# Performance work log

Measured on AMD Instinct MI355X. Metric: run time of the kernel, lower is better.

## Reference

```python
import jax, jax.numpy as jnp
import numpy as np

EMB_DIM = 256
Q_DIM = 512
V_DIM = 512

def setup_inputs() -> dict:
    key = jax.random.key(0)
    ks = jax.random.split(key, 7)
    B, S = 8, 2048
    x = jax.random.normal(ks[0], (B, S, EMB_DIM), dtype=jnp.float32)
    s = 1.0 / np.sqrt(EMB_DIM)
    Wq = jax.random.normal(ks[1], (EMB_DIM, Q_DIM), dtype=jnp.float32) * s
    bq = jax.random.normal(ks[2], (Q_DIM,), dtype=jnp.float32) * 0.01
    Wk = jax.random.normal(ks[3], (EMB_DIM, Q_DIM), dtype=jnp.float32) * s
    bk = jax.random.normal(ks[4], (Q_DIM,), dtype=jnp.float32) * 0.01
    Wv = jax.random.normal(ks[5], (EMB_DIM, V_DIM), dtype=jnp.float32) * s
    bv = jax.random.normal(ks[6], (V_DIM,), dtype=jnp.float32) * 0.01
    return {"x": x, "Wq": Wq, "bq": bq, "Wk": Wk, "bk": bk, "Wv": Wv, "bv": bv}

def reference(x, Wq, bq, Wk, bk, Wv, bv):
    # q/k/v projections (torch Linear == x @ W + b with W stored [in, out] here)
    q = jax.nn.sigmoid(jnp.einsum('bse,eq->bsq', x, Wq) + bq)   # [B,S,Q]
    k = jnp.einsum('bse,eq->bsq', x, Wk) + bk                   # [B,S,Q]
    v = jnp.einsum('bse,ev->bsv', x, Wv) + bv                   # [B,S,V]
    scale = 1.0 / jnp.sqrt(jnp.float32(EMB_DIM))
    qk = jnp.einsum('bsq,btq->bst', q, k) * scale               # [B,S,S]
    qk = jax.nn.elu(qk)
    attn = jax.nn.softmax(qk, axis=-1)
    return jnp.einsum('bst,btv->bsv', attn, v)                  # [B,S,V]
```

## Files before the change

kernel.cpp:

```cpp
#include <hip/hip_runtime.h>
#include <hip/hip_bf16.h>
#include <math.h>

typedef unsigned short u16;
using short8 = __attribute__((ext_vector_type(8))) short;
using f32x4  = __attribute__((ext_vector_type(4))) float;

#define BK 32


__device__ __forceinline__ u16 f2bf(float f) {
  union { float f; unsigned u; } v; v.f = f;
  unsigned r = v.u + 0x7FFFu + ((v.u >> 16) & 1u);
  return (u16)(r >> 16);
}

__device__ __forceinline__ float fexp(float x) { return __expf(x); }

__device__ __forceinline__ void gld16(const void* g, void* l) {
  __builtin_amdgcn_global_load_lds(
      (const __attribute__((address_space(1))) void*)g,
      (__attribute__((address_space(3))) void*)l,
      16, 0, 0);
}


__device__ __forceinline__ void gemm_core64(const u16* __restrict__ Ag,
                                            const u16* __restrict__ Bg,
                                            int K, int lda, int ldb,
                                            u16* As, u16* Bs,
                                            f32x4 acc[4][4], int w, int l) {
  const int wm = (w & 1) << 6, wn = (w >> 1) << 6;
  const int ln = l & 15, lq = l >> 4;
  const int sr0 = w * 16 + (l >> 2);
  const int sr1 = 64 + sr0;
  const int skp = (l & 3) * 8;
  const int skg = ((l & 3) ^ ((l >> 3) & 3)) * 8;
  const int kro = (lq ^ ((ln >> 1) & 3)) * 8;

#pragma unroll
  for (int mt = 0; mt < 4; mt++)
#pragma unroll
    for (int nt = 0; nt < 4; nt++) acc[mt][nt] = (f32x4)0.0f;

  for (int k0 = 0; k0 < K; k0 += 64) {
    __syncthreads();
    gld16(Ag + (size_t)sr0 * lda + k0 + skg, As + sr0 * BK + skp);
    gld16(Ag + (size_t)sr1 * lda + k0 + skg, As + sr1 * BK + skp);
    gld16(Ag + (size_t)sr0 * lda + k0 + 32 + skg, As + 4096 + sr0 * BK + skp);
    gld16(Ag + (size_t)sr1 * lda + k0 + 32 + skg, As + 4096 + sr1 * BK + skp);
    gld16(Bg + (size_t)sr0 * ldb + k0 + skg, Bs + sr0 * BK + skp);
    gld16(Bg + (size_t)sr1 * ldb + k0 + skg, Bs + sr1 * BK + skp);
    gld16(Bg + (size_t)sr0 * ldb + k0 + 32 + skg, Bs + 4096 + sr0 * BK + skp);
    gld16(Bg + (size_t)sr1 * ldb + k0 + 32 + skg, Bs + 4096 + sr1 * BK + skp);
    __syncthreads();
#pragma unroll
    for (int h = 0; h < 2; h++) {
      const u16* Ah = As + h * 4096;
      const u16* Bh = Bs + h * 4096;
      short8 af[4], bf[4];
#pragma unroll
      for (int mt = 0; mt < 4; mt++)
        af[mt] = *(const short8*)(Ah + (wm + mt * 16 + ln) * BK + kro);
#pragma unroll
      for (int nt = 0; nt < 4; nt++)
        bf[nt] = *(const short8*)(Bh + (wn + nt * 16 + ln) * BK + kro);
#pragma unroll
      for (int mt = 0; mt < 4; mt++)
#pragma unroll
        for (int nt = 0; nt < 4; nt++)
          acc[mt][nt] = __builtin_amdgcn_mfma_f32_16x16x32_bf16(
              af[mt], bf[nt], acc[mt][nt], 0, 0, 0);
    }
  }
}


__global__ __launch_bounds__(256) void k_conv(
    const float* __restrict__ Wq, const float* __restrict__ Wk,
    const float* __restrict__ Wv, const float* __restrict__ bq,
    const float* __restrict__ bk, const float* __restrict__ bv,
    u16* __restrict__ Wt, float* __restrict__ bcat,
    float* __restrict__ lsum) {
  const int bid = blockIdx.x;
  if (bid < 1536) {
    int i = bid * 256 + threadIdx.x;
    int nn = i >> 8, e = i & 255;
    int sel = nn >> 9, c = nn & 511;
    const float* W = (sel == 0) ? Wq : (sel == 1) ? Wk : Wv;
    Wt[i] = f2bf(W[e * 512 + c]);
    if (e == 0) {
      const float* bb = (sel == 0) ? bq : (sel == 1) ? bk : bv;
      bcat[nn] = bb[c];
    }
  } else {
    int i = (bid - 1536) * 256 + threadIdx.x;
    lsum[i] = 0.0f;
  }
}


__global__ __launch_bounds__(256) void k_proj(
    const float* __restrict__ x, const u16* __restrict__ Wt,
    const float* __restrict__ bcat, u16* __restrict__ qb,
    u16* __restrict__ kb, u16* __restrict__ vtb) {
  __shared__ __align__(16) u16 As8[8 * 4096];
  __shared__ __align__(16) u16 Bs[2 * 4096];
  const int bm = blockIdx.y * 128;
  const int bnq = blockIdx.x;
  const int tid = threadIdx.x, w = tid >> 6, l = tid & 63;
  const int wm = (w & 1) << 6, wn = (w >> 1) << 6;
  const int ln = l & 15, lq = l >> 4;
  const int sr0 = w * 16 + (l >> 2);
  const int sr1 = 64 + sr0;
  const int skp = (l & 3) * 8;
  const int skg = ((l & 3) ^ ((l >> 3) & 3)) * 8;
  const int kro = (lq ^ ((ln >> 1) & 3)) * 8;

#pragma unroll
  for (int kw = 0; kw < 8; kw++) {
    const f32x4* s0 = (const f32x4*)(x + (size_t)(bm + sr0) * 256 + kw * 32 + skg);
    const f32x4* s1 = (const f32x4*)(x + (size_t)(bm + sr1) * 256 + kw * 32 + skg);
    f32x4 a0 = __builtin_nontemporal_load(s0);
    f32x4 a1 = __builtin_nontemporal_load(s0 + 1);
    f32x4 b0 = __builtin_nontemporal_load(s1);
    f32x4 b1 = __builtin_nontemporal_load(s1 + 1);
    short8 v0, v1;
#pragma unroll
    for (int j = 0; j < 4; j++) {
      ((u16*)&v0)[j]     = f2bf(a0[j]);
      ((u16*)&v0)[4 + j] = f2bf(a1[j]);
      ((u16*)&v1)[j]     = f2bf(b0[j]);
      ((u16*)&v1)[4 + j] = f2bf(b1[j]);
    }
    *(short8*)(As8 + kw * 4096 + sr0 * BK + skp) = v0;
    *(short8*)(As8 + kw * 4096 + sr1 * BK + skp) = v1;
  }

  const int b = bm >> 11, t0 = bm & 2047;
  const int cb = bnq * 128;

  for (int p = 0; p < 3; p++) {
    const u16* Bg = Wt + (size_t)(p * 512 + cb) * 256;
    f32x4 acc[4][4];
#pragma unroll
    for (int mt = 0; mt < 4; mt++)
#pragma unroll
      for (int nt = 0; nt < 4; nt++) acc[mt][nt] = (f32x4)0.0f;

#pragma unroll
    for (int it2 = 0; it2 < 4; it2++) {
      __syncthreads();
      gld16(Bg + (size_t)sr0 * 256 + it2 * 64 + skg, Bs + sr0 * BK + skp);
      gld16(Bg + (size_t)sr1 * 256 + it2 * 64 + skg, Bs + sr1 * BK + skp);
      gld16(Bg + (size_t)sr0 * 256 + it2 * 64 + 32 + skg,
            Bs + 4096 + sr0 * BK + skp);
      gld16(Bg + (size_t)sr1 * 256 + it2 * 64 + 32 + skg,
            Bs + 4096 + sr1 * BK + skp);
      __syncthreads();
#pragma unroll
      for (int h = 0; h < 2; h++) {
        const u16* Aw = As8 + (it2 * 2 + h) * 4096;
        const u16* Bh = Bs + h * 4096;
        short8 af[4], bf[4];
#pragma unroll
        for (int mt = 0; mt < 4; mt++)
          af[mt] = *(const short8*)(Aw + (wm + mt * 16 + ln) * BK + kro);
#pragma unroll
        for (int nt = 0; nt < 4; nt++)
          bf[nt] = *(const short8*)(Bh + (wn + nt * 16 + ln) * BK + kro);
#pragma unroll
        for (int mt = 0; mt < 4; mt++)
#pragma unroll
          for (int nt = 0; nt < 4; nt++)
            acc[mt][nt] = __builtin_amdgcn_mfma_f32_16x16x32_bf16(
                af[mt], bf[nt], acc[mt][nt], 0, 0, 0);
      }
    }

    if (p < 2) {
      u16* dst = p ? kb : qb;
#pragma unroll
      for (int mt = 0; mt < 4; mt++)
#pragma unroll
        for (int r = 0; r < 4; r++) {
          int row = bm + wm + mt * 16 + lq * 4 + r;
          ushort4 o;
#pragma unroll
          for (int nt = 0; nt < 4; nt++) {
            int col = wn + nt * 16 + ln;
            float v = acc[mt][nt][r] + bcat[p * 512 + cb + col];
            float ov = (p == 0) ? __builtin_amdgcn_rcpf(1.0f + fexp(-v)) : v;
            ((u16*)&o)[nt] = f2bf(ov);
          }
          *(ushort4*)&dst[(size_t)row * 512 + cb + wn + ln * 4] = o;
        }
    } else {
      u16* tr = As8;
#pragma unroll
      for (int h = 0; h < 2; h++) {
        __syncthreads();
        if ((w & 1) == h) {
#pragma unroll
          for (int nt = 0; nt < 4; nt++) {
            int c = wn + nt * 16 + ln;
            float bias = bcat[1024 + cb + c];
#pragma unroll
            for (int r = 0; r < 4; r++) {
              ushort4 o;
#pragma unroll
              for (int mm = 0; mm < 4; mm++)
                ((u16*)&o)[mm] = f2bf(acc[mm][nt][r] + bias);
              *(ushort4*)&tr[c * 68 + lq * 16 + r * 4] = o;
            }
          }
        }
        __syncthreads();
        int c2 = tid >> 1, half = tid & 1;
        size_t dbase = ((size_t)b * 512 + cb + c2) * 2048 + t0 + h * 64 + half * 32;
#pragma unroll
        for (int j = 0; j < 4; j++) {
          ushort4 a0 = *(const ushort4*)&tr[c2 * 68 + half * 32 + j * 8];
          ushort4 a1 = *(const ushort4*)&tr[c2 * 68 + half * 32 + j * 8 + 4];
          *(ushort4*)&vtb[dbase + j * 8] = a0;
          *(ushort4*)&vtb[dbase + j * 8 + 4] = a1;
        }
      }
    }
  }
}


__global__ __launch_bounds__(256, 4) void k_qk(const u16* __restrict__ qb,
                                               const u16* __restrict__ kb,
                                               u16* __restrict__ P,
                                               float* __restrict__ lsum) {
  __shared__ __align__(16) u16 As[2 * 4096];
  __shared__ __align__(16) u16 Bs[2 * 4096];
  const int bid = blockIdx.x;
  const int b = bid & 7, t = bid >> 3;
  const int bm = (t >> 4) * 128, bn = (t & 15) * 128;
  const size_t ob = (size_t)b * 2048 * 512;
  const int tid = threadIdx.x, w = tid >> 6, l = tid & 63;
  f32x4 acc[4][4];
  gemm_core64(qb + ob + (size_t)bm * 512, kb + ob + (size_t)bn * 512,
              512, 512, 512, As, Bs, acc, w, l);

  const int wm = (w & 1) << 6, wn = (w >> 1) << 6;
  const int ln = l & 15, lq = l >> 4;
  const float scale = 0.0625f;
#pragma unroll
  for (int mt = 0; mt < 4; mt++)
#pragma unroll
    for (int r = 0; r < 4; r++) {
      int row = bm + wm + mt * 16 + lq * 4 + r;
      float s = 0.0f;
      ushort4 o;
#pragma unroll
      for (int nt = 0; nt < 4; nt++) {
        float v = acc[mt][nt][r] * scale;
        float e = (v > 0.0f) ? v : (fexp(v) - 1.0f);
        float p = fexp(e);
        ((u16*)&o)[nt] = f2bf(p);
        s += p;
      }
      *(ushort4*)&P[((size_t)b * 2048 + row) * 2048 + bn + wn + ln * 4] = o;
#pragma unroll
      for (int o2 = 1; o2 < 16; o2 <<= 1) s += __shfl_xor(s, o2);
      if (ln == 0) atomicAdd(&lsum[b * 2048 + row], s);
    }
}


__global__ __launch_bounds__(256, 4) void k_pv(const u16* __restrict__ P,
                                               const u16* __restrict__ vtb,
                                               const float* __restrict__ lsum,
                                               float* __restrict__ out) {
  __shared__ __align__(16) u16 As[2 * 4096];
  __shared__ __align__(16) u16 Bs[2 * 4096];
  const int bid = blockIdx.x;
  const int b = bid & 7, t = bid >> 3;
  const int bm = (t >> 2) * 128, bn = (t & 3) * 128;
  const int tid = threadIdx.x, w = tid >> 6, l = tid & 63;
  f32x4 acc[4][4];
  gemm_core64(P  + (size_t)b * 2048 * 2048 + (size_t)bm * 2048,
              vtb + (size_t)b * 512 * 2048 + (size_t)bn * 2048,
              2048, 2048, 2048, As, Bs, acc, w, l);

  const int wm = (w & 1) << 6, wn = (w >> 1) << 6;
  const int ln = l & 15, lq = l >> 4;
#pragma unroll
  for (int mt = 0; mt < 4; mt++)
#pragma unroll
    for (int r = 0; r < 4; r++) {
      int row = bm + wm + mt * 16 + lq * 4 + r;
      float inv = 1.0f / lsum[b * 2048 + row];
#pragma unroll
      for (int nt = 0; nt < 4; nt++) {
        int col = bn + wn + nt * 16 + ln;
        out[((size_t)b * 2048 + row) * 512 + col] = acc[mt][nt][r] * inv;
      }
    }
}


extern "C" void kernel_launch(void* const* d_in, const int* in_sizes, int n_in,
                              void* d_out, int out_size, void* d_ws, size_t ws_size,
                              hipStream_t stream) {
  const float* x  = (const float*)d_in[0];
  const float* Wq = (const float*)d_in[1];
  const float* bq = (const float*)d_in[2];
  const float* Wk = (const float*)d_in[3];
  const float* bk = (const float*)d_in[4];
  const float* Wv = (const float*)d_in[5];
  const float* bv = (const float*)d_in[6];
  float* out = (float*)d_out;
  char* ws = (char*)d_ws;

  u16*  qb   = (u16*)(ws + 0);
  u16*  kb   = (u16*)(ws + 16777216);
  u16*  vtb  = (u16*)(ws + 33554432);
  float* lsum = (float*)(ws + 50331648);
  u16*  P    = (u16*)(ws + 50397184);
  u16*  Wt   = (u16*)(ws + 58785792);
  float* bcat = (float*)(ws + 59572224);

  k_conv<<<1600, 256, 0, stream>>>(Wq, Wk, Wv, bq, bk, bv, Wt, bcat, lsum);
  k_proj<<<dim3(4, 128, 1), 256, 0, stream>>>(x, Wt, bcat, qb, kb, vtb);
  k_qk<<<2048, 256, 0, stream>>>(qb, kb, P, lsum);
  k_pv<<<512, 256, 0, stream>>>(P, vtb, lsum, out);
}
```

Baseline: 205.5 us.

## Rewrite QK GEMM with 256x256 tiles, 8 waves and pipelined swizzled LDS staging

The QK^T kernel moves from 128x128 tiles with 4 waves to 256x256 tiles with 8 waves. It uses a hand-scheduled K loop that splits each 64-wide K step into halves and stages the next tile into a second LDS buffer with direct global-to-LDS loads, interleaved between MFMA bursts. Loads are XOR-swizzled to avoid LDS bank conflicts, and s_setprio wraps the MFMA sections. The larger tiles cut global traffic per output, at the cost of 128 KB of LDS and higher register pressure, which limits occupancy to about one block per CU.

```diff
diff --git a/kernel.cpp b/kernel.cpp
--- a/kernel.cpp
+++ b/kernel.cpp
@@ -231,29 +231,126 @@
 }
 
 
-__global__ __launch_bounds__(256, 4) void k_qk(const u16* __restrict__ qb,
+__global__ __launch_bounds__(512, 2) void k_qk(const u16* __restrict__ qb,
                                                const u16* __restrict__ kb,
                                                u16* __restrict__ P,
                                                float* __restrict__ lsum) {
-  __shared__ __align__(16) u16 As[2 * 4096];
-  __shared__ __align__(16) u16 Bs[2 * 4096];
+  __shared__ __align__(16) u16 S[65536];
   const int bid = blockIdx.x;
   const int b = bid & 7, t = bid >> 3;
-  const int bm = (t >> 4) * 128, bn = (t & 15) * 128;
+  const int bm = (t >> 3) * 256, bn = (t & 7) * 256;
   const size_t ob = (size_t)b * 2048 * 512;
-  const int tid = threadIdx.x, w = tid >> 6, l = tid & 63;
-  f32x4 acc[4][4];
-  gemm_core64(qb + ob + (size_t)bm * 512, kb + ob + (size_t)bn * 512,
-              512, 512, 512, As, Bs, acc, w, l);
-
-  const int wm = (w & 1) << 6, wn = (w >> 1) << 6;
+  const u16* Ag = qb + ob + (size_t)bm * 512;
+  const u16* Bg = kb + ob + (size_t)bn * 512;
+  const int tid = threadIdx.x;
+  const int w = tid >> 6, l = tid & 63;
+  const int wm2 = w & 1, wn2 = w >> 1;
   const int ln = l & 15, lq = l >> 4;
+  const int srow = tid >> 2;
+  const int skp = (tid & 3) * 8;
+  const int skg = ((tid & 3) ^ ((tid >> 3) & 3)) * 8;
+  const int kro = (lq ^ ((ln >> 1) & 3)) * 8;
+
+  f32x4 acc[8][4];
+#pragma unroll
+  for (int mt = 0; mt < 8; mt++)
+#pragma unroll
+    for (int nt = 0; nt < 4; nt++) acc[mt][nt] = (f32x4)0.0f;
+
+  auto stageW = [&](const u16* G, int T, int kh, int rh, int nb, int opoff) {
+    gld16(G + (size_t)(rh * 128 + srow) * 512 + T * 64 + kh * 32 + skg,
+          S + nb * 32768 + opoff + (kh * 2 + rh) * 4096 + srow * 32 + skp);
+  };
+
+  stageW(Ag, 0, 0, 0, 0, 0);     stageW(Ag, 0, 0, 1, 0, 0);
+  stageW(Bg, 0, 0, 0, 0, 16384); stageW(Bg, 0, 0, 1, 0, 16384);
+  stageW(Ag, 0, 1, 0, 0, 0);     stageW(Ag, 0, 1, 1, 0, 0);
+  stageW(Bg, 0, 1, 0, 0, 16384); stageW(Bg, 0, 1, 1, 0, 16384);
+
+  for (int T = 0; T < 8; ++T) {
+    const int cur = T & 1, nb = cur ^ 1;
+    const u16* Ab = S + cur * 32768;
+    const u16* Bb = S + cur * 32768 + 16384;
+    const int aw0 = wm2 * 4096;
+    const int brow = ((wn2 & 1) * 64 + ln) * 32;
+    const int bw0 = (wn2 >> 1) * 4096;
+
+    asm volatile("s_waitcnt vmcnt(4)" ::: "memory");
+    __builtin_amdgcn_s_barrier();
+
+    short8 af[8], bf[2];
+#pragma unroll
+    for (int mt = 0; mt < 8; mt++)
+      af[mt] = *(const short8*)(Ab + aw0 + (mt * 16 + ln) * 32 + kro);
+    bf[0] = *(const short8*)(Bb + bw0 + brow + 0 * 512 + kro);
+    bf[1] = *(const short8*)(Bb + bw0 + brow + 1 * 512 + kro);
+    if (T < 7) { stageW(Ag, T + 1, 0, 0, nb, 0); stageW(Ag, T + 1, 0, 1, nb, 0); }
+    __builtin_amdgcn_s_setprio(1);
+#pragma unroll
+    for (int mt = 0; mt < 8; mt++)
+#pragma unroll
+      for (int j = 0; j < 2; j++)
+        acc[mt][j] = __builtin_amdgcn_mfma_f32_16x16x32_bf16(
+            af[mt], bf[j], acc[mt][j], 0, 0, 0);
+    __builtin_amdgcn_s_setprio(0);
+    __builtin_amdgcn_s_barrier();
+
+    bf[0] = *(const short8*)(Bb + bw0 + brow + 2 * 512 + kro);
+    bf[1] = *(const short8*)(Bb + bw0 + brow + 3 * 512 + kro);
+    if (T < 7) { stageW(Bg, T + 1, 0, 0, nb, 16384); stageW(Bg, T + 1, 0, 1, nb, 16384); }
+    __builtin_amdgcn_s_setprio(1);
+#pragma unroll
+    for (int mt = 0; mt < 8; mt++)
+#pragma unroll
+      for (int j = 0; j < 2; j++)
+        acc[mt][2 + j] = __builtin_amdgcn_mfma_f32_16x16x32_bf16(
+            af[mt], bf[j], acc[mt][2 + j], 0, 0, 0);
+    __builtin_amdgcn_s_setprio(0);
+    __builtin_amdgcn_s_barrier();
+
+    if (T < 7) {
+      asm volatile("s_waitcnt vmcnt(4)" ::: "memory");
+    } else {
+      asm volatile("s_waitcnt vmcnt(0)" ::: "memory");
+    }
+    __builtin_amdgcn_s_barrier();
+
+#pragma unroll
+    for (int mt = 0; mt < 8; mt++)
+      af[mt] = *(const short8*)(Ab + 8192 + aw0 + (mt * 16 + ln) * 32 + kro);
+    bf[0] = *(const short8*)(Bb + 8192 + bw0 + brow + 0 * 512 + kro);
+    bf[1] = *(const short8*)(Bb + 8192 + bw0 + brow + 1 * 512 + kro);
+    if (T < 7) { stageW(Ag, T + 1, 1, 0, nb, 0); stageW(Ag, T + 1, 1, 1, nb, 0); }
+    __builtin_amdgcn_s_setprio(1);
+#pragma unroll
+    for (int mt = 0; mt < 8; mt++)
+#pragma unroll
+      for (int j = 0; j < 2; j++)
+        acc[mt][j] = __builtin_amdgcn_mfma_f32_16x16x32_bf16(
+            af[mt], bf[j], acc[mt][j], 0, 0, 0);
+    __builtin_amdgcn_s_setprio(0);
+    __builtin_amdgcn_s_barrier();
+
+    bf[0] = *(const short8*)(Bb + 8192 + bw0 + brow + 2 * 512 + kro);
+    bf[1] = *(const short8*)(Bb + 8192 + bw0 + brow + 3 * 512 + kro);
+    if (T < 7) { stageW(Bg, T + 1, 1, 0, nb, 16384); stageW(Bg, T + 1, 1, 1, nb, 16384); }
+    __builtin_amdgcn_s_setprio(1);
+#pragma unroll
+    for (int mt = 0; mt < 8; mt++)
+#pragma unroll
+      for (int j = 0; j < 2; j++)
+        acc[mt][2 + j] = __builtin_amdgcn_mfma_f32_16x16x32_bf16(
+            af[mt], bf[j], acc[mt][2 + j], 0, 0, 0);
+    __builtin_amdgcn_s_setprio(0);
+    __builtin_amdgcn_s_barrier();
+  }
+
   const float scale = 0.0625f;
 #pragma unroll
-  for (int mt = 0; mt < 4; mt++)
+  for (int mt = 0; mt < 8; mt++)
 #pragma unroll
     for (int r = 0; r < 4; r++) {
-      int row = bm + wm + mt * 16 + lq * 4 + r;
+      int row = bm + wm2 * 128 + mt * 16 + lq * 4 + r;
       float s = 0.0f;
       ushort4 o;
 #pragma unroll
@@ -264,7 +361,7 @@
         ((u16*)&o)[nt] = f2bf(p);
         s += p;
       }
-      *(ushort4*)&P[((size_t)b * 2048 + row) * 2048 + bn + wn + ln * 4] = o;
+      *(ushort4*)&P[((size_t)b * 2048 + row) * 2048 + bn + wn2 * 64 + ln * 4] = o;
 #pragma unroll
       for (int o2 = 1; o2 < 16; o2 <<= 1) s += __shfl_xor(s, o2);
       if (ln == 0) atomicAdd(&lsum[b * 2048 + row], s);
@@ -327,6 +424,6 @@
 
   k_conv<<<1600, 256, 0, stream>>>(Wq, Wk, Wv, bq, bk, bv, Wt, bcat, lsum);
   k_proj<<<dim3(4, 128, 1), 256, 0, stream>>>(x, Wt, bcat, qb, kb, vtb);
-  k_qk<<<2048, 256, 0, stream>>>(qb, kb, P, lsum);
+  k_qk<<<512, 512, 0, stream>>>(qb, kb, P, lsum);
   k_pv<<<512, 256, 0, stream>>>(P, vtb, lsum, out);
 }
```

New measurement: 195.3 us. -4.9%, faster.
